# Performance work log

Measured on AMD Instinct MI355X. Metric: run time of the kernel, lower is better.

Reference implementation:

```python
import math
import jax, jax.numpy as jnp
import numpy as np

N, C, H, W = 32, 64, 96, 96
SHIFT_H, SHIFT_W = 1, -1  # fixed values of the random roll shifts

def _dwconv(x, w, dilation, pad):
    # depthwise conv, x: (n,c,h,w), w: (c,1,kh,kw)
    return jax.lax.conv_general_dilated(
        x, w, window_strides=(1, 1), padding=((pad, pad), (pad, pad)),
        rhs_dilation=(dilation, dilation),
        dimension_numbers=('NCHW', 'OIHW', 'NCHW'),
        feature_group_count=x.shape[1])

def _unfold_1x7_d2(x):
    # F.unfold(x, (1,7), dilation=(1,2), padding=(0,6)) -> (n,c,7,h,w)
    n, c, h, w = x.shape
    xp = jnp.pad(x, ((0, 0), (0, 0), (0, 0), (6, 6)))
    return jnp.stack([xp[..., 2 * k: 2 * k + w] for k in range(7)], axis=2)

def setup_inputs() -> dict:
    key = jax.random.key(0)
    k0, k1, k2, k3, k4, k5 = jax.random.split(key, 6)
    std = 0.1
    return {
        'x':  jax.random.normal(k0, (N, C, H, W), dtype=jnp.float32),
        'w3': jax.random.normal(k1, (C, 1, 5, 5), dtype=jnp.float32) * std,
        'w4': jax.random.normal(k2, (C, 1, 3, 3), dtype=jnp.float32) * std,
        'p5': jax.random.normal(k3, (1, C, C), dtype=jnp.float32) * std,
        'p6': jax.random.normal(k4, (C, 1), dtype=jnp.float32) * std,
        'p8': jax.random.normal(k5, (C, C * 7), dtype=jnp.float32) * std,
    }

def reference(x, w3, w4, p5, p6, p8):
    n, c, h, w = x.shape
    hw = h * w
    t0 = x
    t1 = jnp.roll(jnp.roll(t0, SHIFT_H, axis=2), SHIFT_W, axis=3)
    # channel attention: (n,c,c)
    t2 = jnp.einsum('nci,ndi->ncd', t0.reshape(n, c, hw), t1.reshape(n, c, hw)) / math.sqrt(hw)
    t3 = _dwconv(t1, w3, dilation=1, pad=2)          # (n,c,h,w)
    t4 = _dwconv(t1, w4, dilation=2, pad=2)          # (n,c,h,w)
    t5 = p5 * t2                                      # (n,c,c)
    t6 = jnp.einsum('nchw,ce->nehw', t4, p6).reshape(n, h, w)
    t7 = _unfold_1x7_d2(t0).reshape(n, c * 7, hw)     # (n, c*7, hw)
    t8 = jnp.einsum('nbc,bd->ndc', t5, p8)            # (n, c*7, c)
    t9 = jnp.einsum('nci,ni->nc', t3.reshape(n, c, hw), t6.reshape(n, hw)) / math.sqrt(hw)
    t10 = jnp.einsum('nkc,nks->ncs', t8, t7) / math.sqrt(c * 7)  # (n,c,hw)
    t11 = t9[:, :, None] + t10
    return t11.reshape(n, c, h, w)
```

## Files before the change

kernel.cpp:

```cpp
#include <hip/hip_runtime.h>

#define NB 32
#define CCH 64
#define HH 96
#define WWID 96
#define HWP (HH*WWID)
#define K7 448

#define OFF_T5 2097152
#define OFF_T8 2228224
#define OFF_T6 3145728
#define OFF_T9 3440640

typedef __attribute__((ext_vector_type(8))) short short8;
typedef __attribute__((ext_vector_type(4))) short shortx4;
typedef __attribute__((ext_vector_type(4))) float floatx4;
typedef float __attribute__((ext_vector_type(4), aligned(4))) float4u;

__device__ __forceinline__ short f2bf(float x) {
    unsigned u = __float_as_uint(x);
    unsigned r = (u + 0x7FFF + ((u >> 16) & 1)) >> 16;
    return (short)r;
}

__device__ __forceinline__ void ld_ab(const float* __restrict__ xa, int base,
                                      float4u* va, float4u* vb, int t) {
#pragma unroll
    for (int i = 0; i < 2; i++) {
        int idx = i * 256 + t;
        int c = idx >> 3, k4 = idx & 7;
        int gi = base + k4 * 4;
        const float* xc = xa + c * HWP;
        va[i] = *(const float4u*)(xc + gi);
        int h = gi / WWID, w = gi - h * WWID;
        int hr = (h == 0) ? (HH - 1) : (h - 1);
        const float* xrow = xc + hr * WWID;
        if (w < 92) {
            vb[i] = *(const float4u*)(xrow + w + 1);
        } else {
            float4u tmp;
            tmp.x = xrow[93]; tmp.y = xrow[94]; tmp.z = xrow[95]; tmp.w = xrow[0];
            vb[i] = tmp;
        }
    }
}

__global__ __launch_bounds__(256) void k_t2(const float* __restrict__ x,
                                            float* __restrict__ t2p) {
    int blk = blockIdx.x;
    int n = blk >> 4, sl = blk & 15;
    int k0 = sl * 576;
    __shared__ short ash[64][40];
    __shared__ short bsh[64][40];
    int t = threadIdx.x;
    int lane = t & 63, wv = t >> 6;
    int q = lane >> 4, r16 = lane & 15;
    const float* xa = x + (size_t)n * CCH * HWP;

    floatx4 acc[4] = {};

    float4u va[2], vb[2];
    ld_ab(xa, k0, va, vb, t);

    for (int kc = 0; kc < 576; kc += 32) {
        __syncthreads();
#pragma unroll
        for (int i = 0; i < 2; i++) {
            int idx = i * 256 + t;
            int c = idx >> 3, k4 = idx & 7;
            shortx4 pa = {f2bf(va[i].x), f2bf(va[i].y), f2bf(va[i].z), f2bf(va[i].w)};
            shortx4 pb = {f2bf(vb[i].x), f2bf(vb[i].y), f2bf(vb[i].z), f2bf(vb[i].w)};
            *(shortx4*)&ash[c][k4 * 4] = pa;
            *(shortx4*)&bsh[c][k4 * 4] = pb;
        }
        __syncthreads();
        if (kc + 32 < 576)
            ld_ab(xa, k0 + kc + 32, va, vb, t);
        short8 bfrag = *(const short8*)&bsh[wv * 16 + r16][q * 8];
#pragma unroll
        for (int mi = 0; mi < 4; mi++) {
            short8 afrag = *(const short8*)&ash[mi * 16 + r16][q * 8];
            acc[mi] = __builtin_amdgcn_mfma_f32_16x16x32_bf16(afrag, bfrag, acc[mi], 0, 0, 0);
        }
    }

    float* o = t2p + (size_t)(n * 16 + sl) * 4096;
#pragma unroll
    for (int mi = 0; mi < 4; mi++) {
        int m = mi * 16 + q * 4;
#pragma unroll
        for (int i = 0; i < 4; i++)
            o[(m + i) * 64 + wv * 16 + r16] = acc[mi][i];
    }
}

__global__ __launch_bounds__(256) void k_t5(const float* __restrict__ t2p,
                                            const float* __restrict__ p5,
                                            float* __restrict__ t5) {
    int idx = blockIdx.x * 256 + threadIdx.x;
    int n = idx >> 12, rc = idx & 4095;
    float s = 0.f;
#pragma unroll
    for (int sl = 0; sl < 16; sl++)
        s += t2p[((size_t)n * 16 + sl) * 4096 + rc];
    t5[idx] = s * p5[rc] * (1.0f / 96.0f);
}

__global__ __launch_bounds__(256) void k_t8(const float* __restrict__ t5,
                                            const float* __restrict__ p8,
                                            short* __restrict__ t8t) {
    int n = blockIdx.y;
    int idx = blockIdx.x * 256 + threadIdx.x;
    int k = idx >> 6, c = idx & 63;
    const float* t5n = t5 + (size_t)n * 4096;
    float s = 0.f;
#pragma unroll 8
    for (int b = 0; b < 64; b++)
        s += t5n[b * 64 + c] * p8[b * K7 + k];
    int c7 = k / 7, kk = k - c7 * 7;
    t8t[((size_t)n * 64 + c) * K7 + kk * 64 + c7] = f2bf(s * 0.04724555912f);
}

__global__ __launch_bounds__(256) void k_t6(const float* __restrict__ x,
                                            const float* __restrict__ w4,
                                            const float* __restrict__ p6,
                                            float* __restrict__ t6) {
    int n = blockIdx.y;
    int pix = blockIdx.x * 256 + threadIdx.x;
    int h = pix / WWID, w = pix - h * WWID;

    int off9[9];
    float m9[9];
#pragma unroll
    for (int i = 0; i < 3; i++) {
        int gh = h + (i - 1) * 2;
        bool vr = (gh >= 0) && (gh < HH);
        int srow = vr ? ((gh + HH - 1) % HH) * WWID : 0;
        float rm = vr ? 1.f : 0.f;
#pragma unroll
        for (int j = 0; j < 3; j++) {
            int gw = w + (j - 1) * 2;
            bool vc = (gw >= 0) && (gw < WWID);
            int scol = vc ? (gw + 1) % WWID : 0;
            off9[i * 3 + j] = srow + scol;
            m9[i * 3 + j] = vc ? rm : 0.f;
        }
    }
    const float* xn = x + (size_t)n * CCH * HWP;
    float acc = 0.f;
    for (int c = 0; c < CCH; c++) {
        const float* xc = xn + c * HWP;
        float pw = p6[c];
        const float* wc = w4 + c * 9;
#pragma unroll
        for (int ij = 0; ij < 9; ij++) {
            float wm = wc[ij] * pw * m9[ij];
            acc = fmaf(wm, xc[off9[ij]], acc);
        }
    }
    t6[(size_t)n * HWP + pix] = acc;
}

__global__ __launch_bounds__(256) void k_t9(const float* __restrict__ x,
                                            const float* __restrict__ w3,
                                            const float* __restrict__ t6,
                                            float* __restrict__ t9) {
    int n = blockIdx.y, c = blockIdx.x;
    __shared__ float xl[100][100];
    __shared__ float red[4];
    int t = threadIdx.x;
    const float* xc = x + ((size_t)n * CCH + c) * HWP;
    const float* t6n = t6 + (size_t)n * HWP;

    for (int idx = t; idx < 784; idx += 256) {
        if (idx < 400) {
            int r = idx / 100, col = idx - r * 100;
            int row = r < 2 ? r : r + 96;
            xl[row][col] = 0.f;
        } else {
            int rem = idx - 400;
            int h2 = rem >> 2, c4 = rem & 3;
            int col = c4 < 2 ? c4 : c4 + 96;
            xl[2 + h2][col] = 0.f;
        }
    }
    for (int idx = t; idx < HWP; idx += 256) {
        int h = idx / WWID, w = idx - h * WWID;
        int sh = (h == 0) ? (HH - 1) : (h - 1);
        int sw = (w == WWID - 1) ? 0 : (w + 1);
        xl[h + 2][w + 2] = xc[sh * WWID + sw];
    }
    float wv[25];
#pragma unroll
    for (int i = 0; i < 25; i++) wv[i] = w3[c * 25 + i];
    __syncthreads();

    float acc = 0.f;
#pragma unroll
    for (int g = 0; g < 9; g++) {
        int idx = g * 256 + t;
        int h = idx / 24, wg = idx - h * 24;
        int w0 = wg * 4;
        float4 tv = *(const float4*)(t6n + h * WWID + w0);
        float conv[4] = {0.f, 0.f, 0.f, 0.f};
#pragma unroll
        for (int kh = 0; kh < 5; kh++) {
            float4 ra = *(const float4*)&xl[h + kh][w0];
            float4 rb = *(const float4*)&xl[h + kh][w0 + 4];
            float r[8] = {ra.x, ra.y, ra.z, ra.w, rb.x, rb.y, rb.z, rb.w};
#pragma unroll
            for (int kw = 0; kw < 5; kw++) {
                float wk = wv[kh * 5 + kw];
                conv[0] = fmaf(wk, r[kw],     conv[0]);
                conv[1] = fmaf(wk, r[kw + 1], conv[1]);
                conv[2] = fmaf(wk, r[kw + 2], conv[2]);
                conv[3] = fmaf(wk, r[kw + 3], conv[3]);
            }
        }
        acc = fmaf(conv[0], tv.x, acc);
        acc = fmaf(conv[1], tv.y, acc);
        acc = fmaf(conv[2], tv.z, acc);
        acc = fmaf(conv[3], tv.w, acc);
    }
#pragma unroll
    for (int off = 32; off > 0; off >>= 1) acc += __shfl_down(acc, off, 64);
    if ((t & 63) == 0) red[t >> 6] = acc;
    __syncthreads();
    if (t == 0)
        t9[n * 64 + c] = (red[0] + red[1] + red[2] + red[3]) * (1.0f / 96.0f);
}

__global__ __launch_bounds__(256) void k_out(const float* __restrict__ x,
                                             const short* __restrict__ t8t,
                                             const float* __restrict__ t9,
                                             float* __restrict__ out) {
    int n = blockIdx.y;
    int h0 = blockIdx.x * 2;
    __shared__ short xsh[193 * 64];
    int t = threadIdx.x;

    if (t < 32) ((int*)xsh)[192 * 32 + t] = 0;

    const float* xn = x + (size_t)n * CCH * HWP;
#pragma unroll
    for (int i = 0; i < 12; i++) {
        int idx = i * 256 + t;
        int r = idx / 1536;
        int rem = idx - r * 1536;
        int c7g = rem / 96, w = rem - c7g * 96;
        const float* src = xn + (size_t)(c7g * 4) * HWP + (h0 + r) * WWID + w;
        shortx4 p = {f2bf(src[0]), f2bf(src[HWP]), f2bf(src[2 * HWP]), f2bf(src[3 * HWP])};
        int R = r * 96 + w;
        *(shortx4*)&xsh[R * 64 + ((c7g * 4) ^ ((R & 7) << 3))] = p;
    }
    __syncthreads();

    int lane = t & 63, wv = t >> 6;
    int q = lane >> 4, sl = lane & 15;
    int mh = wv & 1;
    int sh2 = wv >> 1;
    int rbase = sh2 * 96 - 6;
    floatx4 acc[2][6] = {};
    const short* Abase = t8t + (size_t)n * 64 * K7 + (mh * 32 + sl) * K7 + q * 8;

    auto computeB = [&](int kc, const short8* a) {
        int kk = kc >> 6;
        int c7b = (kc & 63) + q * 8;
        int iwb = sl + 2 * kk;
        short8 b[6];
#pragma unroll
        for (int sj = 0; sj < 6; sj++) {
            int iw = sj * 16 + iwb;
            int Rv;
            if (sj == 0)      Rv = (iw >= 6)  ? (rbase + iw) : 192;
            else if (sj == 5) Rv = (iw < 102) ? (rbase + iw) : 192;
            else              Rv = rbase + iw;
            b[sj] = *(const short8*)&xsh[Rv * 64 + (c7b ^ ((Rv & 7) << 3))];
        }
#pragma unroll
        for (int mi = 0; mi < 2; mi++)
#pragma unroll
            for (int sj = 0; sj < 6; sj++)
                acc[mi][sj] = __builtin_amdgcn_mfma_f32_16x16x32_bf16(
                    a[mi], b[sj], acc[mi][sj], 0, 0, 0);
    };

    short8 a0[2], a1[2];
    a0[0] = *(const short8*)(Abase);
    a0[1] = *(const short8*)(Abase + 16 * K7);

    for (int kc = 0; kc < K7; kc += 64) {
        a1[0] = *(const short8*)(Abase + kc + 32);
        a1[1] = *(const short8*)(Abase + 16 * K7 + kc + 32);
        computeB(kc, a0);
        if (kc + 64 < K7) {
            a0[0] = *(const short8*)(Abase + kc + 64);
            a0[1] = *(const short8*)(Abase + 16 * K7 + kc + 64);
        }
        computeB(kc + 32, a1);
    }

    const float* t9n = t9 + n * 64;
#pragma unroll
    for (int mi = 0; mi < 2; mi++) {
#pragma unroll
        for (int i = 0; i < 4; i++) {
            int c = (mh * 2 + mi) * 16 + q * 4 + i;
            float tv = t9n[c];
            float* orow = out + ((size_t)n * CCH + c) * HWP + (h0 + sh2) * WWID;
#pragma unroll
            for (int sj = 0; sj < 6; sj++)
                orow[sj * 16 + sl] = acc[mi][sj][i] + tv;
        }
    }
}

extern "C" void kernel_launch(void* const* d_in, const int* in_sizes, int n_in,
                              void* d_out, int out_size, void* d_ws, size_t ws_size,
                              hipStream_t stream) {
    const float* x  = (const float*)d_in[0];
    const float* w3 = (const float*)d_in[1];
    const float* w4 = (const float*)d_in[2];
    const float* p5 = (const float*)d_in[3];
    const float* p6 = (const float*)d_in[4];
    const float* p8 = (const float*)d_in[5];
    float* out = (float*)d_out;
    float* ws  = (float*)d_ws;

    float* t2p = ws;
    float* t5  = ws + OFF_T5;
    short* t8t = (short*)(ws + OFF_T8);
    float* t6  = ws + OFF_T6;
    float* t9  = ws + OFF_T9;

    k_t2<<<512, 256, 0, stream>>>(x, t2p);
    k_t5<<<512, 256, 0, stream>>>(t2p, p5, t5);
    k_t8<<<dim3(112, 32), 256, 0, stream>>>(t5, p8, t8t);
    k_t6<<<dim3(36, 32), 256, 0, stream>>>(x, w4, p6, t6);
    k_t9<<<dim3(64, 32), 256, 0, stream>>>(x, w3, t6, t9);
    k_out<<<dim3(48, 32), 256, 0, stream>>>(x, t8t, t9, out);
}
```

Measured before the change: 266.6 us.

## Split t2 reduction into more slices and double-buffer LDS tiles

The channel-attention Gram kernel now splits the HW reduction into 32 slices per batch instead of 16, doubling the grid to 1024 blocks. It also double-buffers the LDS tiles and keeps two register prefetch stages in flight, which removes one barrier per iteration. The cost is twice as much partial-sum workspace, a longer reduction in k_t5, and workspace offsets that had to be moved.

```diff
diff --git a/kernel.cpp b/kernel.cpp
--- a/kernel.cpp
+++ b/kernel.cpp
@@ -7,10 +7,10 @@
 #define HWP (HH*WWID)
 #define K7 448
 
-#define OFF_T5 2097152
-#define OFF_T8 2228224
-#define OFF_T6 3145728
-#define OFF_T9 3440640
+#define OFF_T5 4194304
+#define OFF_T8 4325376
+#define OFF_T6 4784128
+#define OFF_T9 5079040
 
 typedef __attribute__((ext_vector_type(8))) short short8;
 typedef __attribute__((ext_vector_type(4))) short shortx4;
@@ -48,10 +48,10 @@
 __global__ __launch_bounds__(256) void k_t2(const float* __restrict__ x,
                                             float* __restrict__ t2p) {
     int blk = blockIdx.x;
-    int n = blk >> 4, sl = blk & 15;
-    int k0 = sl * 576;
-    __shared__ short ash[64][40];
-    __shared__ short bsh[64][40];
+    int n = blk >> 5, sl = blk & 31;
+    int k0 = sl * 288;
+    __shared__ short ash[2][64][40];
+    __shared__ short bsh[2][64][40];
     int t = threadIdx.x;
     int lane = t & 63, wv = t >> 6;
     int q = lane >> 4, r16 = lane & 15;
@@ -59,32 +59,36 @@
 
     floatx4 acc[4] = {};
 
-    float4u va[2], vb[2];
-    ld_ab(xa, k0, va, vb, t);
-
-    for (int kc = 0; kc < 576; kc += 32) {
-        __syncthreads();
+    float4u va[2][2], vb[2][2];
+    ld_ab(xa, k0,      va[0], vb[0], t);
+    ld_ab(xa, k0 + 32, va[1], vb[1], t);
+
+#pragma unroll
+    for (int it = 0; it < 9; it++) {
+        const int cur = it & 1;
 #pragma unroll
         for (int i = 0; i < 2; i++) {
             int idx = i * 256 + t;
             int c = idx >> 3, k4 = idx & 7;
-            shortx4 pa = {f2bf(va[i].x), f2bf(va[i].y), f2bf(va[i].z), f2bf(va[i].w)};
-            shortx4 pb = {f2bf(vb[i].x), f2bf(vb[i].y), f2bf(vb[i].z), f2bf(vb[i].w)};
-            *(shortx4*)&ash[c][k4 * 4] = pa;
-            *(shortx4*)&bsh[c][k4 * 4] = pb;
-        }
+            shortx4 pa = {f2bf(va[cur][i].x), f2bf(va[cur][i].y),
+                          f2bf(va[cur][i].z), f2bf(va[cur][i].w)};
+            shortx4 pb = {f2bf(vb[cur][i].x), f2bf(vb[cur][i].y),
+                          f2bf(vb[cur][i].z), f2bf(vb[cur][i].w)};
+            *(shortx4*)&ash[cur][c][k4 * 4] = pa;
+            *(shortx4*)&bsh[cur][c][k4 * 4] = pb;
+        }
+        if (it + 2 < 9)
+            ld_ab(xa, k0 + (it + 2) * 32, va[cur], vb[cur], t);
         __syncthreads();
-        if (kc + 32 < 576)
-            ld_ab(xa, k0 + kc + 32, va, vb, t);
-        short8 bfrag = *(const short8*)&bsh[wv * 16 + r16][q * 8];
+        short8 bfrag = *(const short8*)&bsh[cur][wv * 16 + r16][q * 8];
 #pragma unroll
         for (int mi = 0; mi < 4; mi++) {
-            short8 afrag = *(const short8*)&ash[mi * 16 + r16][q * 8];
+            short8 afrag = *(const short8*)&ash[cur][mi * 16 + r16][q * 8];
             acc[mi] = __builtin_amdgcn_mfma_f32_16x16x32_bf16(afrag, bfrag, acc[mi], 0, 0, 0);
         }
     }
 
-    float* o = t2p + (size_t)(n * 16 + sl) * 4096;
+    float* o = t2p + (size_t)(n * 32 + sl) * 4096;
 #pragma unroll
     for (int mi = 0; mi < 4; mi++) {
         int m = mi * 16 + q * 4;
@@ -101,8 +105,8 @@
     int n = idx >> 12, rc = idx & 4095;
     float s = 0.f;
 #pragma unroll
-    for (int sl = 0; sl < 16; sl++)
-        s += t2p[((size_t)n * 16 + sl) * 4096 + rc];
+    for (int sl = 0; sl < 32; sl++)
+        s += t2p[((size_t)n * 32 + sl) * 4096 + rc];
     t5[idx] = s * p5[rc] * (1.0f / 96.0f);
 }
 
@@ -333,7 +337,7 @@
     float* t6  = ws + OFF_T6;
     float* t9  = ws + OFF_T9;
 
-    k_t2<<<512, 256, 0, stream>>>(x, t2p);
+    k_t2<<<1024, 256, 0, stream>>>(x, t2p);
     k_t5<<<512, 256, 0, stream>>>(t2p, p5, t5);
     k_t8<<<dim3(112, 32), 256, 0, stream>>>(t5, p8, t8t);
     k_t6<<<dim3(36, 32), 256, 0, stream>>>(x, w4, p6, t6);
```

Measured after the change: 268.1 us. Within noise of the previous version (+0.5%).
